# Kernel tuning notes

Measured on AMD Instinct MI355X. Metric: run time of the kernel, lower is better.

## Reference

```python
import jax, jax.numpy as jnp
import numpy as np

N_NODES = 20000
N_EDGES = 320000
IN_CH = 256
HID_CH = 512


def setup_inputs() -> dict:
    key = jax.random.key(0)
    k_x, k_e, k_w1, k_w2 = jax.random.split(key, 4)
    x = jax.random.normal(k_x, (N_NODES, IN_CH), dtype=jnp.float32)
    edge_index = jax.random.randint(k_e, (2, N_EDGES), 0, N_NODES, dtype=jnp.int32)
    # Glorot-style init for the two GCNConv weight matrices; PyG GCNConv bias init is zeros.
    W1 = jax.random.normal(k_w1, (IN_CH, HID_CH), dtype=jnp.float32) * (1.0 / np.sqrt(IN_CH))
    b1 = jnp.zeros((HID_CH,), dtype=jnp.float32)
    W2 = jax.random.normal(k_w2, (HID_CH, HID_CH), dtype=jnp.float32) * (1.0 / np.sqrt(HID_CH))
    b2 = jnp.zeros((HID_CH,), dtype=jnp.float32)
    return {"x": x, "edge_index": edge_index, "W1": W1, "b1": b1, "W2": W2, "b2": b2}


def _gcn_conv(x, W, b, src, dst, n_nodes):
    """PyG GCNConv: linear transform, then sym-normalized aggregation with self-loops."""
    h = x @ W  # [N, H]
    # in-degree on dst, +1 for the implicit self-loop
    deg = jnp.zeros((n_nodes,), dtype=h.dtype).at[dst].add(1.0) + 1.0
    dinv = jax.lax.rsqrt(deg)  # deg >= 1 always
    norm = dinv[src] * dinv[dst]  # [E]
    msg = h[src] * norm[:, None]  # [E, H] gathered, normalized messages
    agg = jax.ops.segment_sum(msg, dst, num_segments=n_nodes)  # scatter-add to targets
    # self-loop contribution: norm for edge i->i is dinv[i]^2
    return agg + h * (dinv * dinv)[:, None] + b


def reference(x, edge_index, W1, b1, W2, b2):
    src, dst = edge_index[0], edge_index[1]
    n = x.shape[0]
    h = jax.nn.relu(_gcn_conv(x, W1, b1, src, dst, n))
    # dropout(p=0.2) is identity in eval mode
    return _gcn_conv(h, W2, b2, src, dst, n)
```

## Files before the change

kernel.cpp:

```cpp
#include <hip/hip_runtime.h>

#define N_NODES 20000
#define N_EDGES 320000
#define IN_CH 256
#define HID_CH 512
#define NB_SCAN ((N_NODES + 255) / 256)

typedef unsigned short u16;
typedef __attribute__((ext_vector_type(4))) float f32x4;
typedef __attribute__((ext_vector_type(8))) short bf16x8;
typedef __attribute__((ext_vector_type(4))) u16 u16x4;
typedef __attribute__((ext_vector_type(8))) u16 u16x8;

__device__ __forceinline__ float bf2f(u16 h) { return __uint_as_float((unsigned)h << 16); }
__device__ __forceinline__ u16 f2bf(float f) {
    unsigned u = __float_as_uint(f);
    return (u16)((u + 0x7fffu + ((u >> 16) & 1u)) >> 16);
}

__global__ __launch_bounds__(256) void prep_kernel(
        int* __restrict__ deg, int* __restrict__ cursor,
        const float* __restrict__ x, u16* __restrict__ xb,
        const float* __restrict__ W1, u16* __restrict__ hi1,
        const float* __restrict__ W2, u16* __restrict__ hi2) {
    __shared__ float t[64][65];
    int b = blockIdx.x;
    if (b < NB_SCAN) {
        int i = b * 256 + threadIdx.x;
        if (i < N_NODES) { deg[i] = 0; cursor[i] = 0; }
        return;
    }
    b -= NB_SCAN;
    const int XB = N_NODES * IN_CH / 4 / 256;
    if (b < XB) {
        int i = b * 256 + threadIdx.x;
        float4 v = ((const float4*)x)[i];
        u16x4 o = {f2bf(v.x), f2bf(v.y), f2bf(v.z), f2bf(v.w)};
        ((u16x4*)xb)[i] = o;
        return;
    }
    b -= XB;
    const float* W;
    u16* hi;
    int K;
    if (b < 32) { W = W1; hi = hi1; K = IN_CH; }
    else        { b -= 32; W = W2; hi = hi2; K = HID_CH; }
    const int N = HID_CH;
    int k0 = (b >> 3) * 64, n0 = (b & 7) * 64;
    int c = threadIdx.x & 63, r4 = threadIdx.x >> 6;
#pragma unroll
    for (int i = 0; i < 16; ++i) {
        int r = i * 4 + r4;
        t[r][c] = W[(size_t)(k0 + r) * N + n0 + c];
    }
    __syncthreads();
#pragma unroll
    for (int i = 0; i < 16; ++i) {
        int n = i * 4 + r4;
        hi[(size_t)(n0 + n) * K + k0 + c] = f2bf(t[c][n]);
    }
}

__global__ void count_deg_kernel(const int* __restrict__ dst, int* __restrict__ deg, int E) {
    int i = blockIdx.x * blockDim.x + threadIdx.x;
    if (i < E) atomicAdd(&deg[dst[i]], 1);
}

__global__ __launch_bounds__(256) void scan_pass1(const int* __restrict__ deg,
                                                  float* __restrict__ dinv,
                                                  int* __restrict__ bsum, int N) {
    __shared__ int tmp[256];
    int t = threadIdx.x;
    int i = blockIdx.x * 256 + t;
    int d = (i < N) ? deg[i] : 0;
    if (i < N) dinv[i] = rsqrtf((float)d + 1.0f);
    tmp[t] = d;
    __syncthreads();
#pragma unroll
    for (int off = 128; off > 0; off >>= 1) {
        if (t < off) tmp[t] += tmp[t + off];
        __syncthreads();
    }
    if (t == 0) bsum[blockIdx.x] = tmp[0];
}

__global__ __launch_bounds__(256) void scan_pass3(const int* __restrict__ deg,
                                                  const int* __restrict__ bsum,
                                                  int* __restrict__ row_ptr, int N, int E) {
    __shared__ int tmp[256];
    __shared__ int bs[128];
    int t = threadIdx.x;
    if (t < 128) bs[t] = (t < NB_SCAN) ? bsum[t] : 0;
    __syncthreads();
#pragma unroll
    for (int off = 1; off < 128; off <<= 1) {
        int v = (t >= off && t < 128) ? bs[t - off] : 0;
        __syncthreads();
        if (t < 128) bs[t] += v;
        __syncthreads();
    }
    int base = (blockIdx.x == 0) ? 0 : bs[blockIdx.x - 1];
    int i = blockIdx.x * 256 + t;
    int d = (i < N) ? deg[i] : 0;
    tmp[t] = d;
    __syncthreads();
#pragma unroll
    for (int off = 1; off < 256; off <<= 1) {
        int v = (t >= off) ? tmp[t - off] : 0;
        __syncthreads();
        tmp[t] += v;
        __syncthreads();
    }
    if (i < N) row_ptr[i] = base + tmp[t] - d;
    if (i == 0) row_ptr[N] = E;
}

__global__ void scatter_edges_kernel(const int* __restrict__ src, const int* __restrict__ dst,
                                     const int* __restrict__ row_ptr, int* __restrict__ cursor,
                                     const float* __restrict__ dinv, int2* __restrict__ epair,
                                     int E) {
    int e = blockIdx.x * blockDim.x + threadIdx.x;
    if (e >= E) return;
    int d = dst[e];
    int s = src[e];
    int pos = row_ptr[d] + atomicAdd(&cursor[d], 1);
    epair[pos] = make_int2(s, __float_as_int(dinv[s]));
}

template <int C, int SLICES>
__global__ __launch_bounds__(256) void gather_agg_kernel(
        const u16* __restrict__ h, const int2* __restrict__ epair,
        const int* __restrict__ row_ptr, const float* __restrict__ dinv,
        u16* __restrict__ z, int N) {
    int bid = blockIdx.x;
    int nb, s;
    if (SLICES == 8) {
        nb = bid >> 3;
        s = bid & 7;
    } else {
        nb = (bid >> 3) * 2 + (bid & 1);
        s = (bid & 7) >> 1;
    }
    int t = threadIdx.x;
    int grp = t >> 3;
    int u = t & 7;
    int n = nb * 32 + grp;
    bool alive = (n < N);
    int nn = alive ? n : (N - 1);
    float dn = dinv[nn];
    const u16* hbase = h + s * 64 + u * 8;
    float acc[8];
    {
        u16x8 ws = *(const u16x8*)(hbase + (size_t)nn * C);
        float sf = dn * dn;
#pragma unroll
        for (int j = 0; j < 8; ++j) acc[j] = bf2f(ws[j]) * sf;
    }
    int e0 = row_ptr[nn];
    int e1 = alive ? row_ptr[nn + 1] : e0;
    int e = e0;
    for (; e + 8 <= e1; e += 8) {
        int2 p[8];
        u16x8 w[8];
#pragma unroll
        for (int b = 0; b < 8; ++b) p[b] = epair[e + b];
#pragma unroll
        for (int b = 0; b < 8; ++b) w[b] = *(const u16x8*)(hbase + (size_t)p[b].x * C);
#pragma unroll
        for (int b = 0; b < 8; ++b) {
            float nr = __int_as_float(p[b].y) * dn;
#pragma unroll
            for (int j = 0; j < 8; ++j) acc[j] = fmaf(bf2f(w[b][j]), nr, acc[j]);
        }
    }
    for (; e + 4 <= e1; e += 4) {
        int2 p0 = epair[e + 0], p1 = epair[e + 1], p2 = epair[e + 2], p3 = epair[e + 3];
        u16x8 w0 = *(const u16x8*)(hbase + (size_t)p0.x * C);
        u16x8 w1 = *(const u16x8*)(hbase + (size_t)p1.x * C);
        u16x8 w2 = *(const u16x8*)(hbase + (size_t)p2.x * C);
        u16x8 w3 = *(const u16x8*)(hbase + (size_t)p3.x * C);
        float n0 = __int_as_float(p0.y) * dn, n1 = __int_as_float(p1.y) * dn;
        float n2 = __int_as_float(p2.y) * dn, n3 = __int_as_float(p3.y) * dn;
#pragma unroll
        for (int j = 0; j < 8; ++j) {
            acc[j] = fmaf(bf2f(w0[j]), n0, acc[j]);
            acc[j] = fmaf(bf2f(w1[j]), n1, acc[j]);
            acc[j] = fmaf(bf2f(w2[j]), n2, acc[j]);
            acc[j] = fmaf(bf2f(w3[j]), n3, acc[j]);
        }
    }
    for (; e < e1; ++e) {
        int2 p = epair[e];
        u16x8 w = *(const u16x8*)(hbase + (size_t)p.x * C);
        float nr = __int_as_float(p.y) * dn;
#pragma unroll
        for (int j = 0; j < 8; ++j) acc[j] = fmaf(bf2f(w[j]), nr, acc[j]);
    }
    if (alive) {
        u16x8 vh;
#pragma unroll
        for (int j = 0; j < 8; ++j) vh[j] = f2bf(acc[j]);
        *(u16x8*)(z + (size_t)n * C + s * 64 + u * 8) = vh;
    }
}

template <int K, bool RELU, bool OUT_BF16>
__global__ __launch_bounds__(512, 8) void gemm_mfma_kernel(
        const u16* __restrict__ A, const u16* __restrict__ Bh,
        const float* __restrict__ bias, void* __restrict__ Cout, int M, int N) {
    __shared__ u16 lds[2][8192];
    const int tid = threadIdx.x;
    const int lane = tid & 63;
    const int wid = tid >> 6;

    const int nmt = (M + 127) / 128;
    const int total = nmt * 4;
    int bid = blockIdx.x;
    int q = total >> 3, r = total & 7;
    int xcd = bid & 7, pp = bid >> 3;
    int lin = (xcd < r) ? (xcd * (q + 1) + pp) : (r * (q + 1) + (xcd - r) * q + pp);
    const int bm = (lin >> 2) * 128;
    const int bn = (lin & 3) * 128;

    const int wm = (wid & 1) * 64;
    const int wn = (wid >> 1) * 32;

    f32x4 acc[4][2];
#pragma unroll
    for (int i = 0; i < 4; ++i)
#pragma unroll
        for (int j = 0; j < 2; ++j) acc[i][j] = (f32x4){0.f, 0.f, 0.f, 0.f};

    const int srow = (wid << 4) + (lane >> 2);
    const int scb = (((lane & 3) ^ ((lane >> 3) & 3)) << 4);
    const char* srcA  = (const char*)(A  + (size_t)min(bm + srow, M - 1) * K) + scb;
    const char* srcBh = (const char*)(Bh + (size_t)(bn + srow) * K) + scb;
    const int dstoff = wid << 10;

#define GLL(srcp, dstb)                                                                  \
    __builtin_amdgcn_global_load_lds(                                                    \
        (const __attribute__((address_space(1))) void*)(srcp),                           \
        (__attribute__((address_space(3))) void*)((char*)&lds[buf][0] + (dstb)), 16, 0, 0)

#define STAGE(bufv, k0)                                                                  \
    do {                                                                                 \
        int buf = (bufv);                                                                \
        size_t kb2 = (size_t)(k0) * 2;                                                   \
        GLL(srcA + kb2, dstoff);                                                         \
        GLL(srcBh + kb2, 8192 + dstoff);                                                 \
    } while (0)

    STAGE(0, 0);

    const int NT = K / 32;
    const int kb = (lane >> 4) << 4;
#pragma unroll
    for (int t = 0; t < NT; ++t) {
        int cur = t & 1;
        if (t + 1 < NT) {
            STAGE(cur ^ 1, (t + 1) * 32);
            asm volatile("s_waitcnt vmcnt(2)" ::: "memory");
        } else {
            asm volatile("s_waitcnt vmcnt(0)" ::: "memory");
        }
        __builtin_amdgcn_s_barrier();
        asm volatile("" ::: "memory");

        const char* L = (const char*)&lds[cur][0];
        bf16x8 a[4], b_h[2];
#pragma unroll
        for (int i = 0; i < 4; ++i) {
            int ra = wm + i * 16 + (lane & 15);
            int off = ra * 64 + (kb ^ (((ra >> 1) & 3) << 4));
            a[i] = *(const bf16x8*)(L + off);
        }
#pragma unroll
        for (int j = 0; j < 2; ++j) {
            int rb = wn + j * 16 + (lane & 15);
            int off = rb * 64 + (kb ^ (((rb >> 1) & 3) << 4));
            b_h[j] = *(const bf16x8*)(L + 8192 + off);
        }
#pragma unroll
        for (int i = 0; i < 4; ++i)
#pragma unroll
            for (int j = 0; j < 2; ++j)
                acc[i][j] = __builtin_amdgcn_mfma_f32_16x16x32_bf16(a[i], b_h[j], acc[i][j], 0, 0, 0);
        asm volatile("" ::: "memory");
        __builtin_amdgcn_s_barrier();
    }
#undef STAGE
#undef GLL

#pragma unroll
    for (int j = 0; j < 2; ++j) {
        int gc = bn + wn + j * 16 + (lane & 15);
        float bv = bias[gc];
#pragma unroll
        for (int i = 0; i < 4; ++i) {
#pragma unroll
            for (int t = 0; t < 4; ++t) {
                int gr = bm + wm + i * 16 + ((lane >> 4) << 2) + t;
                if (gr < M) {
                    float v = acc[i][j][t] + bv;
                    if (RELU) v = fmaxf(v, 0.f);
                    if (OUT_BF16)
                        ((u16*)Cout)[(size_t)gr * N + gc] = f2bf(v);
                    else
                        ((float*)Cout)[(size_t)gr * N + gc] = v;
                }
            }
        }
    }
}

extern "C" void kernel_launch(void* const* d_in, const int* in_sizes, int n_in,
                              void* d_out, int out_size, void* d_ws, size_t ws_size,
                              hipStream_t stream) {
    const float* x  = (const float*)d_in[0];
    const int*   ei = (const int*)d_in[1];
    const float* W1 = (const float*)d_in[2];
    const float* b1 = (const float*)d_in[3];
    const float* W2 = (const float*)d_in[4];
    const float* b2 = (const float*)d_in[5];
    const int* src = ei;
    const int* dst = ei + N_EDGES;

    char* ws = (char*)d_ws;
    size_t off = 0;
    auto alloc = [&](size_t bytes) {
        void* p = ws + off;
        off = (off + bytes + 255) & ~(size_t)255;
        return p;
    };
    int*   deg     = (int*)alloc(N_NODES * 4);
    int*   cursor  = (int*)alloc(N_NODES * 4);
    int*   row_ptr = (int*)alloc((N_NODES + 1) * 4);
    float* dinv    = (float*)alloc(N_NODES * 4);
    int*   bsum    = (int*)alloc(NB_SCAN * 4);
    int2*  epair   = (int2*)alloc((size_t)N_EDGES * 8);
    u16*   wt1_hi  = (u16*)alloc((size_t)IN_CH * HID_CH * 2);
    u16*   wt2_hi  = (u16*)alloc((size_t)HID_CH * HID_CH * 2);
    u16*   xb      = (u16*)alloc((size_t)N_NODES * IN_CH * 2);
    u16*   z1      = (u16*)alloc((size_t)N_NODES * IN_CH * 2);
    u16*   z2      = (u16*)alloc((size_t)N_NODES * HID_CH * 2);
    u16*   h1      = (u16*)d_out;

    const int XB = N_NODES * IN_CH / 4 / 256;
    prep_kernel<<<NB_SCAN + XB + 96, 256, 0, stream>>>(deg, cursor, x, xb, W1, wt1_hi, W2,
                                                       wt2_hi);
    count_deg_kernel<<<(N_EDGES + 255) / 256, 256, 0, stream>>>(dst, deg, N_EDGES);
    scan_pass1<<<NB_SCAN, 256, 0, stream>>>(deg, dinv, bsum, N_NODES);
    scan_pass3<<<NB_SCAN, 256, 0, stream>>>(deg, bsum, row_ptr, N_NODES, N_EDGES);
    scatter_edges_kernel<<<(N_EDGES + 255) / 256, 256, 0, stream>>>(src, dst, row_ptr, cursor,
                                                                    dinv, epair, N_EDGES);

    const int NMT = (N_NODES + 127) / 128;
    const int NB32 = (N_NODES + 31) / 32;
    gather_agg_kernel<IN_CH, 4><<<((NB32 + 1) / 2) * 8, 256, 0, stream>>>(
        xb, epair, row_ptr, dinv, z1, N_NODES);
    gemm_mfma_kernel<IN_CH, true, true><<<NMT * 4, 512, 0, stream>>>(z1, wt1_hi, b1, h1,
                                                                     N_NODES, HID_CH);

    gather_agg_kernel<HID_CH, 8><<<NB32 * 8, 256, 0, stream>>>(
        h1, epair, row_ptr, dinv, z2, N_NODES);
    gemm_mfma_kernel<HID_CH, false, false><<<NMT * 4, 512, 0, stream>>>(z2, wt2_hi, b2,
                                                                        (float*)d_out, N_NODES,
                                                                        HID_CH);
}
```

Before: 145.0 us.

## Merge degree counting into conversion kernel and use single-pass decoupled scan

The degree-count atomics are folded into the same launch as the bf16 conversion of x and the weight transposes, and zeroing moves to a small kernel of its own. The two-pass block scan becomes a single kernel in which each block publishes its total with a release flag and spins on the flags of earlier blocks. This removes one launch overall and overlaps the atomics with the conversion work. The spin-wait depends on all 79 blocks being co-resident, which holds on this GPU but is a forward-progress assumption.

```diff
diff --git a/kernel.cpp b/kernel.cpp
--- a/kernel.cpp
+++ b/kernel.cpp
@@ -5,6 +5,7 @@
 #define IN_CH 256
 #define HID_CH 512
 #define NB_SCAN ((N_NODES + 255) / 256)
+#define EB ((N_EDGES + 255) / 256)
 
 typedef unsigned short u16;
 typedef __attribute__((ext_vector_type(4))) float f32x4;
@@ -18,19 +19,26 @@
     return (u16)((u + 0x7fffu + ((u >> 16) & 1u)) >> 16);
 }
 
-__global__ __launch_bounds__(256) void prep_kernel(
-        int* __restrict__ deg, int* __restrict__ cursor,
+__global__ void zero_kernel(int* __restrict__ deg, int* __restrict__ cursor,
+                            int* __restrict__ flag, int n, int nf) {
+    int i = blockIdx.x * blockDim.x + threadIdx.x;
+    if (i < n) { deg[i] = 0; cursor[i] = 0; }
+    if (i < nf) flag[i] = 0;
+}
+
+__global__ __launch_bounds__(256) void count_convert_kernel(
+        const int* __restrict__ dst, int* __restrict__ deg,
         const float* __restrict__ x, u16* __restrict__ xb,
         const float* __restrict__ W1, u16* __restrict__ hi1,
         const float* __restrict__ W2, u16* __restrict__ hi2) {
     __shared__ float t[64][65];
     int b = blockIdx.x;
-    if (b < NB_SCAN) {
+    if (b < EB) {
         int i = b * 256 + threadIdx.x;
-        if (i < N_NODES) { deg[i] = 0; cursor[i] = 0; }
+        if (i < N_EDGES) atomicAdd(&deg[dst[i]], 1);
         return;
     }
-    b -= NB_SCAN;
+    b -= EB;
     const int XB = N_NODES * IN_CH / 4 / 256;
     if (b < XB) {
         int i = b * 256 + threadIdx.x;
@@ -61,47 +69,15 @@
     }
 }
 
-__global__ void count_deg_kernel(const int* __restrict__ dst, int* __restrict__ deg, int E) {
-    int i = blockIdx.x * blockDim.x + threadIdx.x;
-    if (i < E) atomicAdd(&deg[dst[i]], 1);
-}
-
-__global__ __launch_bounds__(256) void scan_pass1(const int* __restrict__ deg,
-                                                  float* __restrict__ dinv,
-                                                  int* __restrict__ bsum, int N) {
+__global__ __launch_bounds__(256) void scan_one_kernel(
+        const int* __restrict__ deg, float* __restrict__ dinv, int* __restrict__ row_ptr,
+        int* __restrict__ agg, int* __restrict__ flag, int N, int E) {
     __shared__ int tmp[256];
-    int t = threadIdx.x;
-    int i = blockIdx.x * 256 + t;
+    __shared__ int part[256];
+    int t = threadIdx.x, b = blockIdx.x;
+    int i = b * 256 + t;
     int d = (i < N) ? deg[i] : 0;
     if (i < N) dinv[i] = rsqrtf((float)d + 1.0f);
-    tmp[t] = d;
-    __syncthreads();
-#pragma unroll
-    for (int off = 128; off > 0; off >>= 1) {
-        if (t < off) tmp[t] += tmp[t + off];
-        __syncthreads();
-    }
-    if (t == 0) bsum[blockIdx.x] = tmp[0];
-}
-
-__global__ __launch_bounds__(256) void scan_pass3(const int* __restrict__ deg,
-                                                  const int* __restrict__ bsum,
-                                                  int* __restrict__ row_ptr, int N, int E) {
-    __shared__ int tmp[256];
-    __shared__ int bs[128];
-    int t = threadIdx.x;
-    if (t < 128) bs[t] = (t < NB_SCAN) ? bsum[t] : 0;
-    __syncthreads();
-#pragma unroll
-    for (int off = 1; off < 128; off <<= 1) {
-        int v = (t >= off && t < 128) ? bs[t - off] : 0;
-        __syncthreads();
-        if (t < 128) bs[t] += v;
-        __syncthreads();
-    }
-    int base = (blockIdx.x == 0) ? 0 : bs[blockIdx.x - 1];
-    int i = blockIdx.x * 256 + t;
-    int d = (i < N) ? deg[i] : 0;
     tmp[t] = d;
     __syncthreads();
 #pragma unroll
@@ -111,6 +87,25 @@
         tmp[t] += v;
         __syncthreads();
     }
+    if (t == 255) {
+        __hip_atomic_store(&agg[b], tmp[255], __ATOMIC_RELAXED, __HIP_MEMORY_SCOPE_AGENT);
+        __hip_atomic_store(&flag[b], 1, __ATOMIC_RELEASE, __HIP_MEMORY_SCOPE_AGENT);
+    }
+    int v = 0;
+    if (t < b) {
+        while (__hip_atomic_load(&flag[t], __ATOMIC_ACQUIRE, __HIP_MEMORY_SCOPE_AGENT) == 0) {
+            __builtin_amdgcn_s_sleep(8);
+        }
+        v = __hip_atomic_load(&agg[t], __ATOMIC_RELAXED, __HIP_MEMORY_SCOPE_AGENT);
+    }
+    part[t] = v;
+    __syncthreads();
+#pragma unroll
+    for (int off = 128; off > 0; off >>= 1) {
+        if (t < off) part[t] += part[t + off];
+        __syncthreads();
+    }
+    int base = part[0];
     if (i < N) row_ptr[i] = base + tmp[t] - d;
     if (i == 0) row_ptr[N] = E;
 }
@@ -336,7 +331,8 @@
     int*   cursor  = (int*)alloc(N_NODES * 4);
     int*   row_ptr = (int*)alloc((N_NODES + 1) * 4);
     float* dinv    = (float*)alloc(N_NODES * 4);
-    int*   bsum    = (int*)alloc(NB_SCAN * 4);
+    int*   agg     = (int*)alloc(NB_SCAN * 4);
+    int*   flag    = (int*)alloc(NB_SCAN * 4);
     int2*  epair   = (int2*)alloc((size_t)N_EDGES * 8);
     u16*   wt1_hi  = (u16*)alloc((size_t)IN_CH * HID_CH * 2);
     u16*   wt2_hi  = (u16*)alloc((size_t)HID_CH * HID_CH * 2);
@@ -345,14 +341,14 @@
     u16*   z2      = (u16*)alloc((size_t)N_NODES * HID_CH * 2);
     u16*   h1      = (u16*)d_out;
 
+    zero_kernel<<<NB_SCAN, 256, 0, stream>>>(deg, cursor, flag, N_NODES, NB_SCAN);
     const int XB = N_NODES * IN_CH / 4 / 256;
-    prep_kernel<<<NB_SCAN + XB + 96, 256, 0, stream>>>(deg, cursor, x, xb, W1, wt1_hi, W2,
-                                                       wt2_hi);
-    count_deg_kernel<<<(N_EDGES + 255) / 256, 256, 0, stream>>>(dst, deg, N_EDGES);
-    scan_pass1<<<NB_SCAN, 256, 0, stream>>>(deg, dinv, bsum, N_NODES);
-    scan_pass3<<<NB_SCAN, 256, 0, stream>>>(deg, bsum, row_ptr, N_NODES, N_EDGES);
-    scatter_edges_kernel<<<(N_EDGES + 255) / 256, 256, 0, stream>>>(src, dst, row_ptr, cursor,
-                                                                    dinv, epair, N_EDGES);
+    count_convert_kernel<<<EB + XB + 96, 256, 0, stream>>>(dst, deg, x, xb, W1, wt1_hi, W2,
+                                                           wt2_hi);
+    scan_one_kernel<<<NB_SCAN, 256, 0, stream>>>(deg, dinv, row_ptr, agg, flag, N_NODES,
+                                                 N_EDGES);
+    scatter_edges_kernel<<<EB, 256, 0, stream>>>(src, dst, row_ptr, cursor, dinv, epair,
+                                                 N_EDGES);
 
     const int NMT = (N_NODES + 127) / 128;
     const int NB32 = (N_NODES + 31) / 32;
```

Measured after the change: 149.8 us. +3.4%, slower.
